# Kernel tuning notes

Hardware: AMD Instinct MI355X
Metric: run time of the kernel (lower is better)

The kernel has to match this reference:

```python
import jax, jax.numpy as jnp
import numpy as np

B, PANO, OBJ, CFG, LM, IMG, D = 64, 36, 36, 16, 8, 32, 300
H, EMB, ANG, FEAT = 512, 64, 128, 2176
TOPN = 3
EPS = 1e-8


def setup_inputs() -> dict:
    key = jax.random.key(0)
    ks = jax.random.split(key, 24)
    f = lambda i, shape: jax.random.normal(ks[i], shape, dtype=jnp.float32)
    u = lambda i, shape: jax.random.uniform(ks[i], shape, dtype=jnp.float32)
    s = 0.02
    return {
        "action": f(0, (B, ANG)),
        "feature": f(1, (B, PANO, FEAT)),
        "cand_feat": f(2, (B, IMG, FEAT)),
        "prev_h1": f(3, (B, H)),
        "c_0": f(4, (B, H)),
        "ctx": f(5, (B, CFG, H)),
        "s_0": u(6, (B, CFG)),
        "landmark_object_feature": f(7, (B, CFG, LM, D)),
        "candidate_obj_text_feat": f(8, (B, IMG, OBJ, D)),
        "landmark_mask": u(9, (B, CFG, LM)),
        "landmark_relation": f(10, (B, CFG, LM, 6)),
        "landmark_relation_mask": u(11, (B, CFG, LM)),
        "candidate_relation": f(12, (B, IMG, 6)),
        "pano_obj_feat": f(13, (B, PANO, OBJ, D)),
        "emb_W": f(14, (ANG, EMB)) * s,
        "emb_b": jnp.zeros((EMB,), jnp.float32),
        "W_ih": f(15, (EMB + FEAT + TOPN * D, 4 * H)) * s,
        "W_hh": f(16, (H, 4 * H)) * s,
        "b_lstm": jnp.zeros((4 * H,), jnp.float32),
        "feat_in_W": f(17, (H, FEAT + TOPN * D)) * s,
        "att_in_W": f(18, (H, H)) * s,
        "att_out_W": f(19, (2 * H, H)) * s,
        "cand_in_W": f(20, (H, FEAT + TOPN * 7 + TOPN * D)) * s,
        "ctx_mask": jnp.zeros((B, CFG), dtype=bool),
    }


def _cos_argmax(obj_feat, land_flat):
    # obj_feat: [B,I,O,D], land_flat: [B,M,D] -> argmax over O of cosine sim: [B,I,M]
    dot = jnp.einsum('biod,bmd->biom', obj_feat, land_flat)
    na = jnp.linalg.norm(obj_feat, axis=-1)
    nb = jnp.linalg.norm(land_flat, axis=-1)
    sim = dot / jnp.maximum(na[..., None] * nb[:, None, None, :], EPS)
    return jnp.argmax(sim, axis=2)


def reference(action, feature, cand_feat, prev_h1, c_0, ctx, s_0,
              landmark_object_feature, candidate_obj_text_feat, landmark_mask,
              landmark_relation, landmark_relation_mask, candidate_relation,
              pano_obj_feat, emb_W, emb_b, W_ih, W_hh, b_lstm, feat_in_W,
              att_in_W, att_out_W, cand_in_W, ctx_mask):
    M = CFG * LM
    land_flat = landmark_object_feature.reshape(B, M, D)

    # --- pano object retrieval (cosine argmax + top-N config*landmark gather) ---
    pano_idx = _cos_argmax(pano_obj_feat, land_flat)                   # [B,36,M]
    top_idx = jax.lax.top_k((s_0[..., None] * landmark_mask).reshape(B, M), TOPN)[1]  # [B,3]
    sel = jnp.take_along_axis(pano_idx, jnp.broadcast_to(top_idx[:, None, :], (B, PANO, TOPN)), axis=2)
    pano_sim_obj = jnp.take_along_axis(
        pano_obj_feat, jnp.broadcast_to(sel[..., None], (B, PANO, TOPN, D)), axis=2
    ).reshape(B, PANO, TOPN * D)

    # --- embed action, feature attention (dropout = identity in eval) ---
    action_embeds = jnp.tanh(action @ emb_W + emb_b)
    feat_all = jnp.concatenate([feature, pano_sim_obj], axis=-1)       # [B,36,FEAT+900]
    a = jnp.einsum('bsd,bd->bs', feat_all, prev_h1 @ feat_in_W)
    p = jax.nn.softmax(a, axis=-1)
    attn_feat = jnp.einsum('bs,bsd->bd', p, feat_all)

    # --- LSTM cell ---
    gates = jnp.concatenate([action_embeds, attn_feat], axis=-1) @ W_ih + prev_h1 @ W_hh + b_lstm
    i_g, f_g, g_g, o_g = jnp.split(gates, 4, axis=-1)
    c_1 = jax.nn.sigmoid(f_g) * c_0 + jax.nn.sigmoid(i_g) * jnp.tanh(g_g)
    h_1 = jax.nn.sigmoid(o_g) * jnp.tanh(c_1)

    # --- ctx attention with mask + tilde ---
    lg = jnp.einsum('bsd,bd->bs', ctx, h_1 @ att_in_W)
    lg = jnp.where(ctx_mask, -jnp.inf, lg)
    ctx_attn = jax.nn.softmax(lg, axis=-1)
    wctx = jnp.einsum('bs,bsd->bd', ctx_attn, ctx)
    h_tilde = jnp.tanh(jnp.concatenate([wctx, h_1], axis=-1) @ att_out_W)

    # --- candidate object retrieval ---
    cand_idx = _cos_argmax(candidate_obj_text_feat, land_flat)         # [B,IMG,M]
    ctop = jax.lax.top_k((ctx_attn[..., None] * landmark_mask).reshape(B, M), TOPN)[1]
    land_rel_top = jnp.take_along_axis(landmark_relation.reshape(B, M, 6),
                                       jnp.broadcast_to(ctop[..., None], (B, TOPN, 6)), axis=1)
    land_obj_rel = jnp.einsum('bik,bjk->bij', candidate_relation, land_rel_top)   # [B,IMG,3]
    rel_mask_top = jnp.take_along_axis(landmark_relation_mask.reshape(B, M), ctop, axis=1)  # [B,3]
    csel = jnp.take_along_axis(cand_idx, jnp.broadcast_to(ctop[:, None, :], (B, IMG, TOPN)), axis=2)
    candi_sim_obj = jnp.take_along_axis(
        candidate_obj_text_feat, jnp.broadcast_to(csel[..., None], (B, IMG, TOPN, D)), axis=2)
    candi_rel = candidate_relation[:, :, None, :] * rel_mask_top[:, None, :, None]  # [B,IMG,3,6]
    new_feat = jnp.concatenate(
        [candi_sim_obj, jnp.concatenate([candi_rel, land_obj_rel[..., None]], axis=-1)],
        axis=-1).reshape(B, IMG, TOPN * (D + 7))
    cand_all = jnp.concatenate([cand_feat, new_feat], axis=-1)

    logit = jnp.einsum('bsd,bd->bs', cand_all, h_tilde @ cand_in_W)
    return h_1, c_1, logit, h_tilde, ctx_attn
```

## Files before the change

kernel.cpp:

```cpp
#include <hip/hip_runtime.h>
#include <math.h>

#define B_    64
#define PANO_ 36
#define OBJ_  36
#define CFG_  16
#define LM_   8
#define IMG_  32
#define D_    300
#define H_    512
#define EMB_  64
#define ANG_  128
#define FEAT_ 2176
#define M_    128

__device__ __forceinline__ float sigmoidf(float x) { return 1.0f / (1.0f + expf(-x)); }
__device__ __forceinline__ float dot4(float4 a, float4 b) {
    return a.x * b.x + a.y * b.y + a.z * b.z + a.w * b.w;
}
__device__ __forceinline__ float4 add4(float4 a, float4 b) {
    return make_float4(a.x + b.x, a.y + b.y, a.z + b.z, a.w + b.w);
}
__device__ __forceinline__ float4 fma4(float s, float4 a, float4 acc) {
    return make_float4(acc.x + s * a.x, acc.y + s * a.y, acc.z + s * a.z, acc.w + s * a.w);
}
__device__ __forceinline__ float4 ld4(const float* p) { return *reinterpret_cast<const float4*>(p); }

template <int TWO_SEG, int VEC_B>
__global__ __launch_bounds__(256)
void gemm_part(const float* __restrict__ A0, int lda0, int K0, const float* __restrict__ W0,
               const float* __restrict__ A1, int lda1, int K1, const float* __restrict__ W1,
               float* __restrict__ part, int N, int kchunk) {
    __shared__ __align__(16) float As[64][36];
    __shared__ __align__(16) float Bs[32][68];
    const int K = K0 + (TWO_SEG ? K1 : 0);
    int n0 = blockIdx.x * 64;
    int k0 = blockIdx.y * kchunk;
    if (k0 >= K) return;
    int kend = min(K, k0 + kchunk);
    int tid = threadIdx.x;
    int tr = tid >> 4, tc = tid & 15;
    float4 rA4[2];
    float4 rB4[2];
    float rB[8];
    float acc[4][4] = {};

    auto loadA = [&](int kb) {
#pragma unroll
        for (int l = 0; l < 2; l++) {
            int idx = tid + 256 * l;
            int r = idx >> 3, kq = idx & 7;
            int k = kb + 4 * kq;
            float4 v = make_float4(0.f, 0.f, 0.f, 0.f);
            if (k < kend) {
                const float* src = (TWO_SEG && k >= K0)
                    ? A1 + (size_t)r * lda1 + (k - K0)
                    : A0 + (size_t)r * lda0 + k;
                v = ld4(src);
            }
            rA4[l] = v;
        }
    };
    auto loadB = [&](int kb) {
        if (VEC_B) {
#pragma unroll
            for (int l = 0; l < 2; l++) {
                int idx = tid + 256 * l;
                int kk = idx >> 4, c4 = idx & 15;
                int k = kb + kk, n = n0 + 4 * c4;
                float4 v = make_float4(0.f, 0.f, 0.f, 0.f);
                if (k < kend && n < N) {
                    const float* src = (TWO_SEG && k >= K0)
                        ? W1 + (size_t)(k - K0) * N + n
                        : W0 + (size_t)k * N + n;
                    v = ld4(src);
                }
                rB4[l] = v;
            }
        } else {
#pragma unroll
            for (int l = 0; l < 8; l++) {
                int idx = tid + 256 * l;
                int kk = idx >> 6, c = idx & 63;
                int k = kb + kk, n = n0 + c;
                float v = 0.f;
                if (k < kend && n < N) {
                    v = (TWO_SEG && k >= K0) ? W1[(size_t)(k - K0) * N + n]
                                             : W0[(size_t)k * N + n];
                }
                rB[l] = v;
            }
        }
    };
    auto storeLDS = [&]() {
#pragma unroll
        for (int l = 0; l < 2; l++) {
            int idx = tid + 256 * l;
            *reinterpret_cast<float4*>(&As[idx >> 3][4 * (idx & 7)]) = rA4[l];
        }
        if (VEC_B) {
#pragma unroll
            for (int l = 0; l < 2; l++) {
                int idx = tid + 256 * l;
                *reinterpret_cast<float4*>(&Bs[idx >> 4][4 * (idx & 15)]) = rB4[l];
            }
        } else {
#pragma unroll
            for (int l = 0; l < 8; l++) {
                int idx = tid + 256 * l;
                Bs[idx >> 6][idx & 63] = rB[l];
            }
        }
    };
    auto compute = [&]() {
#pragma unroll
        for (int kk0 = 0; kk0 < 32; kk0 += 4) {
            float4 a0 = ld4(&As[4 * tr + 0][kk0]);
            float4 a1 = ld4(&As[4 * tr + 1][kk0]);
            float4 a2 = ld4(&As[4 * tr + 2][kk0]);
            float4 a3 = ld4(&As[4 * tr + 3][kk0]);
            float4 b0 = ld4(&Bs[kk0 + 0][4 * tc]);
            float4 b1 = ld4(&Bs[kk0 + 1][4 * tc]);
            float4 b2 = ld4(&Bs[kk0 + 2][4 * tc]);
            float4 b3 = ld4(&Bs[kk0 + 3][4 * tc]);
#define ROWFMA(i, ai) \
            acc[i][0] += ai.x * b0.x + ai.y * b1.x + ai.z * b2.x + ai.w * b3.x; \
            acc[i][1] += ai.x * b0.y + ai.y * b1.y + ai.z * b2.y + ai.w * b3.y; \
            acc[i][2] += ai.x * b0.z + ai.y * b1.z + ai.z * b2.z + ai.w * b3.z; \
            acc[i][3] += ai.x * b0.w + ai.y * b1.w + ai.z * b2.w + ai.w * b3.w;
            ROWFMA(0, a0) ROWFMA(1, a1) ROWFMA(2, a2) ROWFMA(3, a3)
#undef ROWFMA
        }
    };

    loadA(k0); loadB(k0);
    storeLDS();
    __syncthreads();
    for (int kb = k0 + 32; kb < kend; kb += 32) {
        loadA(kb); loadB(kb);
        compute();
        __syncthreads();
        storeLDS();
        __syncthreads();
    }
    compute();

    float* outp = part + (size_t)blockIdx.y * 64 * N;
    if (VEC_B) {
#pragma unroll
        for (int i = 0; i < 4; i++) {
            int r = 4 * tr + i;
            int n = n0 + 4 * tc;
            if (n < N)
                *reinterpret_cast<float4*>(outp + (size_t)r * N + n) =
                    make_float4(acc[i][0], acc[i][1], acc[i][2], acc[i][3]);
        }
    } else {
#pragma unroll
        for (int i = 0; i < 4; i++) {
            int r = 4 * tr + i;
#pragma unroll
            for (int j = 0; j < 4; j++) {
                int n = n0 + 4 * tc + j;
                if (n < N) outp[(size_t)r * N + n] = acc[i][j];
            }
        }
    }
}

__global__ void reduce4_top3_kernel(const float4* __restrict__ part, int S, int total4,
                                    float4* __restrict__ out,
                                    const float* __restrict__ s0,
                                    const float* __restrict__ lmask,
                                    int* __restrict__ pmids) {
    int tid = threadIdx.x;
    if (blockIdx.x < 193) {
        int i = blockIdx.x * 256 + tid;
        if (i >= total4) return;
        float4 v = make_float4(0.f, 0.f, 0.f, 0.f);
        for (int s = 0; s < S; s++) v = add4(v, part[(size_t)s * total4 + i]);
        out[i] = v;
        return;
    }
    __shared__ float redV[2];
    __shared__ int redI[2];
    __shared__ int mids[3];
    int b = blockIdx.x - 193;
    int wave = tid >> 6, lane = tid & 63;
    float tv; int tm;
    if (tid < 128) { tv = s0[b * CFG_ + (tid >> 3)] * lmask[(size_t)b * M_ + tid]; tm = tid; }
    else { tv = -INFINITY; tm = 1 << 30; }
    for (int t = 0; t < 3; t++) {
        float bv = tv; int bi = tm;
        for (int off = 32; off >= 1; off >>= 1) {
            float ov = __shfl_xor(bv, off);
            int   oi = __shfl_xor(bi, off);
            if (ov > bv || (ov == bv && oi < bi)) { bv = ov; bi = oi; }
        }
        if (lane == 0 && wave < 2) { redV[wave] = bv; redI[wave] = bi; }
        __syncthreads();
        if (tid == 0) {
            int pick = (redV[0] > redV[1] || (redV[0] == redV[1] && redI[0] < redI[1])) ? redI[0] : redI[1];
            mids[t] = pick;
            pmids[b * 3 + t] = pick;
        }
        __syncthreads();
        if (tm == mids[t]) tv = -INFINITY;
    }
}

__global__ void reduce_remap_kernel(const float* __restrict__ part, int S,
                                    float* __restrict__ out) {
    int b = blockIdx.y;
    int c = blockIdx.x * 256 + threadIdx.x;
    if (c >= 3097) return;
    float v = 0.f;
    for (int s = 0; s < S; s++) v += part[(size_t)s * (B_ * 3097) + (size_t)b * 3097 + c];
    int oc;
    if (c < 2176) oc = c;
    else { int u = c - 2176; oc = 2176 + (u / 307) * 308 + (u % 307); }
    out[(size_t)b * 3104 + oc] = v;
}

__global__ void tanh_reduce_kernel(const float4* __restrict__ part, int S,
                                   float4* __restrict__ htld, float4* __restrict__ out_ht) {
    int i = blockIdx.x * 256 + threadIdx.x;
    if (i >= B_ * H_ / 4) return;
    float4 v = make_float4(0.f, 0.f, 0.f, 0.f);
    for (int s = 0; s < S; s++) v = add4(v, part[(size_t)s * (B_ * H_ / 4) + i]);
    float4 t = make_float4(tanhf(v.x), tanhf(v.y), tanhf(v.z), tanhf(v.w));
    htld[i] = t;
    out_ht[i] = t;
}

template <typename F>
__device__ __forceinline__ void cos_phase(int tid, const float* __restrict__ obase,
                                          const float land3[3][304], float simv[3][40],
                                          F&& dotBranch) {
    if (tid < 192) {
        int g = tid >> 2, gl = tid & 3;
        if (g < 36) {
            const float* row = obase + (size_t)g * 300;
            float c0 = 0, c1 = 0, c2 = 0, sn = 0;
            float4 buf[4];
#pragma unroll
            for (int p = 0; p < 4; p++) buf[p] = ld4(row + 4 * (gl + 4 * p));
#pragma unroll
            for (int j = 0; j < 19; j++) {
                int k4 = gl + 4 * j;
                if (k4 < 75) {
                    float4 cur = buf[j & 3];
                    int kn = gl + 4 * (j + 4);
                    if (kn < 75) buf[j & 3] = ld4(row + 4 * kn);
                    float4 l0 = ld4(&land3[0][4 * k4]);
                    float4 l1 = ld4(&land3[1][4 * k4]);
                    float4 l2 = ld4(&land3[2][4 * k4]);
                    sn += dot4(cur, cur);
                    c0 += dot4(cur, l0);
                    c1 += dot4(cur, l1);
                    c2 += dot4(cur, l2);
                }
            }
#pragma unroll
            for (int off = 1; off <= 2; off <<= 1) {
                c0 += __shfl_xor(c0, off);
                c1 += __shfl_xor(c1, off);
                c2 += __shfl_xor(c2, off);
                sn += __shfl_xor(sn, off);
            }
            if (gl == 0) {
                float inv = 1.0f / sqrtf(fmaxf(sn, 1e-20f));
                simv[0][g] = c0 * inv;
                simv[1][g] = c1 * inv;
                simv[2][g] = c2 * inv;
            }
        }
    } else {
        dotBranch(tid - 192);
    }
}

__global__ __launch_bounds__(256)
void pano_logits_kernel(const float* __restrict__ pobj,
                        const float* __restrict__ land,
                        const int* __restrict__ pmids,
                        const float* __restrict__ feature,
                        const float* __restrict__ qfeat,
                        int* __restrict__ sel,
                        float* __restrict__ aval) {
    __shared__ __align__(16) float land3[3][304];
    __shared__ int mids[3];
    __shared__ float simv[3][40];
    __shared__ int fin[3];
    __shared__ float wred[4];
    int i = blockIdx.x, b = blockIdx.y, tid = threadIdx.x;
    int wave = tid >> 6, lane = tid & 63;

    if (tid < 3) mids[tid] = pmids[b * 3 + tid];
    __syncthreads();
    for (int idx = tid; idx < 912; idx += 256) {
        int t = idx / 304, k = idx % 304;
        land3[t][k] = (k < 300) ? land[((size_t)b * 128 + mids[t]) * 300 + k] : 0.f;
    }
    __syncthreads();

    const float* obase = pobj + (((size_t)b * 36 + i) * 36) * 300;
    const float* qf = qfeat + (size_t)b * 3076;
    const float* frow = feature + ((size_t)b * 36 + i) * 2176;
    float facc = 0.f;

    cos_phase(tid, obase, land3, simv, [&](int l) {
#pragma unroll
        for (int j = 0; j < 9; j++) {
            int d4 = l + 64 * j;
            if (d4 < 544)
                facc += dot4(ld4(frow + 4 * d4), ld4(qf + 4 * d4));
        }
    });
    __syncthreads();
    if (tid < 3) {
        float bv = -INFINITY; int bo = 0;
        for (int o2 = 0; o2 < 36; o2++) {
            float v = simv[tid][o2];
            if (v > bv) { bv = v; bo = o2; }
        }
        fin[tid] = bo;
        sel[((size_t)b * 36 + i) * 3 + tid] = bo;
    }
    __syncthreads();

    float acc = facc;
    for (int idx = tid; idx < 225; idx += 256) {
        int t = idx / 75, k4 = idx % 75;
        acc += dot4(ld4(obase + (size_t)fin[t] * 300 + 4 * k4),
                    ld4(qf + 2176 + t * 300 + 4 * k4));
    }
    for (int off = 32; off >= 1; off >>= 1) acc += __shfl_xor(acc, off);
    if (lane == 0) wred[wave] = acc;
    __syncthreads();
    if (tid == 0) aval[b * 36 + i] = wred[0] + wred[1] + wred[2] + wred[3];
}

__global__ __launch_bounds__(256)
void attn_wsum_kernel(const float* __restrict__ feature,
                      const float* __restrict__ pobj,
                      const int* __restrict__ sel,
                      const float* __restrict__ aval,
                      const float* __restrict__ action,
                      const float* __restrict__ embW,
                      const float* __restrict__ embB,
                      float* __restrict__ xcat) {
    __shared__ float lg[36];
    __shared__ float pe[36];
    __shared__ int ss[36][3];
    int b = blockIdx.y, tid = threadIdx.x;
    int d4 = blockIdx.x * 256 + tid;
    if (tid < 36) lg[tid] = aval[b * 36 + tid];
    for (int idx = tid; idx < 108; idx += 256) ss[idx / 3][idx % 3] = sel[(size_t)b * 108 + idx];
    __syncthreads();
    float mx = -INFINITY;
    for (int s = 0; s < 36; s++) mx = fmaxf(mx, lg[s]);
    if (tid < 36) pe[tid] = expf(lg[tid] - mx);
    __syncthreads();
    float sum = 0;
    for (int s = 0; s < 36; s++) sum += pe[s];
    float invS = 1.0f / sum;
    if (d4 < 769) {
        float4 acc = make_float4(0.f, 0.f, 0.f, 0.f);
        if (d4 < 544) {
            const float* fb = feature + (size_t)b * 36 * 2176 + 4 * d4;
#pragma unroll 4
            for (int s = 0; s < 36; s++) acc = fma4(pe[s], ld4(fb + (size_t)s * 2176), acc);
        } else {
            int u = d4 - 544, t = u / 75, k4 = u % 75;
            const float* pb = pobj + (size_t)b * 36 * 36 * 300;
#pragma unroll 4
            for (int s = 0; s < 36; s++)
                acc = fma4(pe[s], ld4(pb + ((size_t)s * 36 + ss[s][t]) * 300 + 4 * k4), acc);
        }
        acc = make_float4(acc.x * invS, acc.y * invS, acc.z * invS, acc.w * invS);
        *reinterpret_cast<float4*>(xcat + (size_t)b * 3140 + 64 + 4 * d4) = acc;
    }
    if (blockIdx.x == 0 && tid < 64) {
        float acc = embB[tid];
        for (int k = 0; k < ANG_; k++)
            acc += action[b * ANG_ + k] * embW[k * EMB_ + tid];
        xcat[(size_t)b * 3140 + tid] = tanhf(acc);
    }
}

__global__ void lstm_kernel(const float* __restrict__ gp, int S,
                            const float* __restrict__ b_lstm,
                            const float* __restrict__ c0,
                            float* __restrict__ out_h1,
                            float* __restrict__ out_c1) {
    int idx4 = blockIdx.x * 256 + threadIdx.x;
    if (idx4 >= B_ * H_ / 4) return;
    int b = idx4 >> 7;
    int d4 = idx4 & 127;
    float4 ig = ld4(b_lstm + 4 * d4);
    float4 fg = ld4(b_lstm + 512 + 4 * d4);
    float4 gg = ld4(b_lstm + 1024 + 4 * d4);
    float4 og = ld4(b_lstm + 1536 + 4 * d4);
    for (int s = 0; s < S; s++) {
        const float* g = gp + (size_t)s * (B_ * 2048) + (size_t)b * 2048 + 4 * d4;
        ig = add4(ig, ld4(g));
        fg = add4(fg, ld4(g + 512));
        gg = add4(gg, ld4(g + 1024));
        og = add4(og, ld4(g + 1536));
    }
    float4 cv = ld4(c0 + 4 * idx4);
    float4 c1, h1;
    c1.x = sigmoidf(fg.x) * cv.x + sigmoidf(ig.x) * tanhf(gg.x);
    c1.y = sigmoidf(fg.y) * cv.y + sigmoidf(ig.y) * tanhf(gg.y);
    c1.z = sigmoidf(fg.z) * cv.z + sigmoidf(ig.z) * tanhf(gg.z);
    c1.w = sigmoidf(fg.w) * cv.w + sigmoidf(ig.w) * tanhf(gg.w);
    h1.x = sigmoidf(og.x) * tanhf(c1.x);
    h1.y = sigmoidf(og.y) * tanhf(c1.y);
    h1.z = sigmoidf(og.z) * tanhf(c1.z);
    h1.w = sigmoidf(og.w) * tanhf(c1.w);
    *reinterpret_cast<float4*>(out_c1 + 4 * idx4) = c1;
    *reinterpret_cast<float4*>(out_h1 + 4 * idx4) = h1;
}

__global__ __launch_bounds__(256)
void ctx_attn_kernel(const float* __restrict__ ctx,
                     const float* __restrict__ qctx_part,
                     const float* __restrict__ h1f,
                     const float* __restrict__ lmask,
                     float* __restrict__ ccbuf,
                     float* __restrict__ out_attn,
                     int* __restrict__ ctop) {
    __shared__ __align__(16) float qc[512];
    __shared__ float part[16][17];
    __shared__ float lgv[16];
    __shared__ float att[16];
    __shared__ float redV[2];
    __shared__ int redI[2];
    __shared__ int mids[3];
    int b = blockIdx.x, tid = threadIdx.x;
    int wave = tid >> 6, lane = tid & 63;
    if (tid < 128) {
        float4 v = make_float4(0.f, 0.f, 0.f, 0.f);
#pragma unroll
        for (int s = 0; s < 8; s++)
            v = add4(v, ld4(qctx_part + (size_t)s * (B_ * 512) + (size_t)b * 512 + 4 * tid));
        *reinterpret_cast<float4*>(&qc[4 * tid]) = v;
    }
    __syncthreads();
    int s = tid >> 4, l = tid & 15;
    float acc = 0;
    for (int d = l; d < 512; d += 16) acc += ctx[((size_t)b * 16 + s) * 512 + d] * qc[d];
    part[s][l] = acc;
    __syncthreads();
    if (tid < 16) {
        float sum = 0;
        for (int j = 0; j < 16; j++) sum += part[tid][j];
        lgv[tid] = sum;
    }
    __syncthreads();
    if (tid < 16) {
        float mx = -INFINITY;
        for (int j = 0; j < 16; j++) mx = fmaxf(mx, lgv[j]);
        att[tid] = expf(lgv[tid] - mx);
    }
    __syncthreads();
    float sum = 0;
    for (int j = 0; j < 16; j++) sum += att[j];
    float invS = 1.0f / sum;
    if (tid < 16) out_attn[b * 16 + tid] = att[tid] * invS;
    for (int d = tid; d < 512; d += 256) {
        float acc2 = 0;
        for (int sj = 0; sj < 16; sj++)
            acc2 += att[sj] * ctx[((size_t)b * 16 + sj) * 512 + d];
        ccbuf[(size_t)b * 1024 + d] = acc2 * invS;
        ccbuf[(size_t)b * 1024 + 512 + d] = h1f[(size_t)b * 512 + d];
    }
    float tv; int tm;
    if (tid < 128) { tv = att[tid >> 3] * lmask[(size_t)b * M_ + tid]; tm = tid; }
    else { tv = -INFINITY; tm = 1 << 30; }
    for (int t = 0; t < 3; t++) {
        float bv = tv; int bi = tm;
        for (int off = 32; off >= 1; off >>= 1) {
            float ov = __shfl_xor(bv, off);
            int   oi = __shfl_xor(bi, off);
            if (ov > bv || (ov == bv && oi < bi)) { bv = ov; bi = oi; }
        }
        if (lane == 0 && wave < 2) { redV[wave] = bv; redI[wave] = bi; }
        __syncthreads();
        if (tid == 0) {
            int pick = (redV[0] > redV[1] || (redV[0] == redV[1] && redI[0] < redI[1])) ? redI[0] : redI[1];
            mids[t] = pick;
            ctop[b * 3 + t] = pick;
        }
        __syncthreads();
        if (tm == mids[t]) tv = -INFINITY;
    }
}

__global__ __launch_bounds__(256)
void cand_fused_kernel(const float* __restrict__ cobj,
                       const float* __restrict__ land,
                       const int* __restrict__ ctop,
                       const float* __restrict__ landrel,
                       const float* __restrict__ lrmask,
                       const float* __restrict__ crel_g,
                       const float* __restrict__ cand_feat,
                       const float* __restrict__ qcand,
                       float* __restrict__ out_logit) {
    __shared__ __align__(16) float land3[3][304];
    __shared__ float relL[3][6];
    __shared__ float relM[3];
    __shared__ float crel[6];
    __shared__ int mids[3];
    __shared__ float simv[3][40];
    __shared__ int fin[3];
    __shared__ float wsum[4];
    int img = blockIdx.x, b = blockIdx.y, tid = threadIdx.x;
    int wave = tid >> 6, lane = tid & 63;
    if (tid < 3) mids[tid] = ctop[b * 3 + tid];
    __syncthreads();
    for (int idx = tid; idx < 912; idx += 256) {
        int t = idx / 304, k = idx % 304;
        land3[t][k] = (k < 300) ? land[((size_t)b * 128 + mids[t]) * 300 + k] : 0.f;
    }
    if (tid < 18) { int t = tid / 6, k = tid % 6; relL[t][k] = landrel[((size_t)b * 128 + mids[t]) * 6 + k]; }
    if (tid >= 32 && tid < 35) { int t = tid - 32; relM[t] = lrmask[(size_t)b * 128 + mids[t]]; }
    if (tid >= 64 && tid < 70) { crel[tid - 64] = crel_g[((size_t)b * 32 + img) * 6 + (tid - 64)]; }
    __syncthreads();

    const float* obase = cobj + (((size_t)b * 32 + img) * 36) * 300;
    const float* q = qcand + (size_t)b * 3104;
    const float* cf = cand_feat + ((size_t)b * 32 + img) * 2176;
    float facc = 0.f;

    cos_phase(tid, obase, land3, simv, [&](int l) {
#pragma unroll
        for (int j = 0; j < 9; j++) {
            int d4 = l + 64 * j;
            if (d4 < 544)
                facc += dot4(ld4(cf + 4 * d4), ld4(q + 4 * d4));
        }
    });
    __syncthreads();
    if (tid < 3) {
        float bv = -INFINITY; int bo = 0;
        for (int o2 = 0; o2 < 36; o2++) {
            float v = simv[tid][o2];
            if (v > bv) { bv = v; bo = o2; }
        }
        fin[tid] = bo;
    }
    __syncthreads();

    float acc = facc;
    for (int idx = tid; idx < 225; idx += 256) {
        int t = idx / 75, k4 = idx % 75;
        acc += dot4(ld4(obase + (size_t)fin[t] * 300 + 4 * k4),
                    ld4(q + 2176 + t * 308 + 4 * k4));
    }
    if (tid < 21) {
        int t = tid / 7, j = tid % 7;
        float val;
        if (j < 6) val = crel[j] * relM[t];
        else { val = 0; for (int k = 0; k < 6; k++) val += crel[k] * relL[t][k]; }
        acc += val * q[2176 + t * 308 + 300 + j];
    }
    for (int off = 32; off >= 1; off >>= 1) acc += __shfl_xor(acc, off);
    if (lane == 0) wsum[wave] = acc;
    __syncthreads();
    if (tid == 0) {
        out_logit[(size_t)b * 32 + img] = wsum[0] + wsum[1] + wsum[2] + wsum[3];
    }
}

extern "C" void kernel_launch(void* const* d_in, const int* in_sizes, int n_in,
                              void* d_out, int out_size, void* d_ws, size_t ws_size,
                              hipStream_t stream) {
    const float* action    = (const float*)d_in[0];
    const float* feature   = (const float*)d_in[1];
    const float* cand_feat = (const float*)d_in[2];
    const float* prev_h1   = (const float*)d_in[3];
    const float* c_0       = (const float*)d_in[4];
    const float* ctx       = (const float*)d_in[5];
    const float* s_0       = (const float*)d_in[6];
    const float* lobj      = (const float*)d_in[7];
    const float* cobj      = (const float*)d_in[8];
    const float* lmask     = (const float*)d_in[9];
    const float* lrel      = (const float*)d_in[10];
    const float* lrelmask  = (const float*)d_in[11];
    const float* crel      = (const float*)d_in[12];
    const float* pobj      = (const float*)d_in[13];
    const float* embW      = (const float*)d_in[14];
    const float* embB      = (const float*)d_in[15];
    const float* W_ih      = (const float*)d_in[16];
    const float* W_hh      = (const float*)d_in[17];
    const float* b_lstm    = (const float*)d_in[18];
    const float* feat_in_W = (const float*)d_in[19];
    const float* att_in_W  = (const float*)d_in[20];
    const float* att_out_W = (const float*)d_in[21];
    const float* cand_in_W = (const float*)d_in[22];

    float* ws = (float*)d_ws;
    float* gates_part = ws;
    float* qf_part    = gates_part + 2621440;
    float* q_feat     = qf_part + 1574912;
    float* qctx_part  = q_feat + 196864;
    float* htpre_part = qctx_part + 262144;
    float* htld       = htpre_part + 524288;
    float* qcand_part = htld + 32768;
    float* q_cand     = qcand_part + 1585664;
    float* xcat       = q_cand + 198656;
    float* ccbuf      = xcat + 200960;
    float* aval       = ccbuf + 65536;
    int*   ctop       = (int*)(aval + 2304);
    int*   sel        = ctop + 192;
    int*   pmids      = sel + 6912;

    float* out       = (float*)d_out;
    float* out_h1    = out;
    float* out_c1    = out + 32768;
    float* out_logit = out + 65536;
    float* out_ht    = out + 67584;
    float* out_attn  = out + 100352;

    gemm_part<0, 1><<<dim3(49, 8), 256, 0, stream>>>(prev_h1, H_, H_, feat_in_W,
                                                     nullptr, 0, 0, nullptr,
                                                     qf_part, 3076, 64);
    reduce4_top3_kernel<<<257, 256, 0, stream>>>((const float4*)qf_part, 8, 49216,
                                                 (float4*)q_feat, s_0, lmask, pmids);

    pano_logits_kernel<<<dim3(PANO_, B_), 256, 0, stream>>>(pobj, lobj, pmids, feature, q_feat, sel, aval);

    attn_wsum_kernel<<<dim3(4, B_), 256, 0, stream>>>(feature, pobj, sel, aval, action, embW, embB, xcat);

    gemm_part<1, 1><<<dim3(32, 20), 256, 0, stream>>>(xcat, 3140, 3140, W_ih,
                                                      prev_h1, H_, H_, W_hh,
                                                      gates_part, 2048, 192);
    lstm_kernel<<<32, 256, 0, stream>>>(gates_part, 20, b_lstm, c_0, out_h1, out_c1);

    gemm_part<0, 1><<<dim3(8, 8), 256, 0, stream>>>(out_h1, H_, H_, att_in_W,
                                                    nullptr, 0, 0, nullptr,
                                                    qctx_part, H_, 64);
    ctx_attn_kernel<<<B_, 256, 0, stream>>>(ctx, qctx_part, out_h1, lmask, ccbuf, out_attn, ctop);

    gemm_part<0, 1><<<dim3(8, 16), 256, 0, stream>>>(ccbuf, 1024, 1024, att_out_W,
                                                     nullptr, 0, 0, nullptr,
                                                     htpre_part, H_, 64);
    tanh_reduce_kernel<<<32, 256, 0, stream>>>((const float4*)htpre_part, 16,
                                               (float4*)htld, (float4*)out_ht);

    gemm_part<0, 0><<<dim3(49, 8), 256, 0, stream>>>(htld, H_, H_, cand_in_W,
                                                     nullptr, 0, 0, nullptr,
                                                     qcand_part, 3097, 64);
    reduce_remap_kernel<<<dim3(13, B_), 256, 0, stream>>>(qcand_part, 8, q_cand);

    cand_fused_kernel<<<dim3(IMG_, B_), 256, 0, stream>>>(cobj, lobj, ctop, lrel, lrelmask,
                                                          crel, cand_feat, q_cand, out_logit);
}
```

Measured before the change: 488.8 us.

## Stage object tile in shared memory with coalesced loads for cosine argmax

Both the pano and candidate logit kernels now copy the whole 36x300 object-feature block into a padded shared-memory tile using all threads with coalesced float4 loads. The cosine similarity and the later gather of the selected objects then read from LDS instead of global memory. The feature dot product that used to overlap in the spare warp is moved after the argmax and spread across all threads. The roughly 44 KB of LDS per block may reduce occupancy, and the feature loads are no longer overlapped with the cosine phase.

```diff
diff --git a/kernel.cpp b/kernel.cpp
--- a/kernel.cpp
+++ b/kernel.cpp
@@ -233,53 +233,6 @@
     out_ht[i] = t;
 }
 
-template <typename F>
-__device__ __forceinline__ void cos_phase(int tid, const float* __restrict__ obase,
-                                          const float land3[3][304], float simv[3][40],
-                                          F&& dotBranch) {
-    if (tid < 192) {
-        int g = tid >> 2, gl = tid & 3;
-        if (g < 36) {
-            const float* row = obase + (size_t)g * 300;
-            float c0 = 0, c1 = 0, c2 = 0, sn = 0;
-            float4 buf[4];
-#pragma unroll
-            for (int p = 0; p < 4; p++) buf[p] = ld4(row + 4 * (gl + 4 * p));
-#pragma unroll
-            for (int j = 0; j < 19; j++) {
-                int k4 = gl + 4 * j;
-                if (k4 < 75) {
-                    float4 cur = buf[j & 3];
-                    int kn = gl + 4 * (j + 4);
-                    if (kn < 75) buf[j & 3] = ld4(row + 4 * kn);
-                    float4 l0 = ld4(&land3[0][4 * k4]);
-                    float4 l1 = ld4(&land3[1][4 * k4]);
-                    float4 l2 = ld4(&land3[2][4 * k4]);
-                    sn += dot4(cur, cur);
-                    c0 += dot4(cur, l0);
-                    c1 += dot4(cur, l1);
-                    c2 += dot4(cur, l2);
-                }
-            }
-#pragma unroll
-            for (int off = 1; off <= 2; off <<= 1) {
-                c0 += __shfl_xor(c0, off);
-                c1 += __shfl_xor(c1, off);
-                c2 += __shfl_xor(c2, off);
-                sn += __shfl_xor(sn, off);
-            }
-            if (gl == 0) {
-                float inv = 1.0f / sqrtf(fmaxf(sn, 1e-20f));
-                simv[0][g] = c0 * inv;
-                simv[1][g] = c1 * inv;
-                simv[2][g] = c2 * inv;
-            }
-        }
-    } else {
-        dotBranch(tid - 192);
-    }
-}
-
 __global__ __launch_bounds__(256)
 void pano_logits_kernel(const float* __restrict__ pobj,
                         const float* __restrict__ land,
@@ -288,6 +241,7 @@
                         const float* __restrict__ qfeat,
                         int* __restrict__ sel,
                         float* __restrict__ aval) {
+    __shared__ __align__(16) float tile[36][308];
     __shared__ __align__(16) float land3[3][304];
     __shared__ int mids[3];
     __shared__ float simv[3][40];
@@ -298,25 +252,43 @@
 
     if (tid < 3) mids[tid] = pmids[b * 3 + tid];
     __syncthreads();
-    for (int idx = tid; idx < 912; idx += 256) {
-        int t = idx / 304, k = idx % 304;
-        land3[t][k] = (k < 300) ? land[((size_t)b * 128 + mids[t]) * 300 + k] : 0.f;
-    }
-    __syncthreads();
-
+
+    for (int q = tid; q < 225; q += 256) {
+        int t = q / 75, k4 = q % 75;
+        *reinterpret_cast<float4*>(&land3[t][4 * k4]) =
+            ld4(land + ((size_t)b * 128 + mids[t]) * 300 + 4 * k4);
+    }
     const float* obase = pobj + (((size_t)b * 36 + i) * 36) * 300;
-    const float* qf = qfeat + (size_t)b * 3076;
-    const float* frow = feature + ((size_t)b * 36 + i) * 2176;
-    float facc = 0.f;
-
-    cos_phase(tid, obase, land3, simv, [&](int l) {
-#pragma unroll
-        for (int j = 0; j < 9; j++) {
-            int d4 = l + 64 * j;
-            if (d4 < 544)
-                facc += dot4(ld4(frow + 4 * d4), ld4(qf + 4 * d4));
-        }
-    });
+    for (int q = tid; q < 2700; q += 256) {
+        int o = q / 75, k4 = q % 75;
+        *reinterpret_cast<float4*>(&tile[o][4 * k4]) = ld4(obase + (size_t)o * 300 + 4 * k4);
+    }
+    __syncthreads();
+
+    int g = tid >> 2, gl = tid & 3;
+    if (g < 36) {
+        float c0 = 0, c1 = 0, c2 = 0, sn = 0;
+        for (int k4 = gl; k4 < 75; k4 += 4) {
+            float4 a = ld4(&tile[g][4 * k4]);
+            sn += dot4(a, a);
+            c0 += dot4(a, ld4(&land3[0][4 * k4]));
+            c1 += dot4(a, ld4(&land3[1][4 * k4]));
+            c2 += dot4(a, ld4(&land3[2][4 * k4]));
+        }
+#pragma unroll
+        for (int off = 1; off <= 2; off <<= 1) {
+            c0 += __shfl_xor(c0, off);
+            c1 += __shfl_xor(c1, off);
+            c2 += __shfl_xor(c2, off);
+            sn += __shfl_xor(sn, off);
+        }
+        if (gl == 0) {
+            float inv = 1.0f / sqrtf(fmaxf(sn, 1e-20f));
+            simv[0][g] = c0 * inv;
+            simv[1][g] = c1 * inv;
+            simv[2][g] = c2 * inv;
+        }
+    }
     __syncthreads();
     if (tid < 3) {
         float bv = -INFINITY; int bo = 0;
@@ -329,11 +301,14 @@
     }
     __syncthreads();
 
-    float acc = facc;
-    for (int idx = tid; idx < 225; idx += 256) {
-        int t = idx / 75, k4 = idx % 75;
-        acc += dot4(ld4(obase + (size_t)fin[t] * 300 + 4 * k4),
-                    ld4(qf + 2176 + t * 300 + 4 * k4));
+    const float* qf = qfeat + (size_t)b * 3076;
+    const float* frow = feature + ((size_t)b * 36 + i) * 2176;
+    float acc = 0;
+    for (int d4 = tid; d4 < 544; d4 += 256)
+        acc += dot4(ld4(frow + 4 * d4), ld4(qf + 4 * d4));
+    for (int q = tid; q < 225; q += 256) {
+        int t = q / 75, k4 = q % 75;
+        acc += dot4(ld4(&tile[fin[t]][4 * k4]), ld4(qf + 2176 + t * 300 + 4 * k4));
     }
     for (int off = 32; off >= 1; off >>= 1) acc += __shfl_xor(acc, off);
     if (lane == 0) wred[wave] = acc;
@@ -508,6 +483,7 @@
                        const float* __restrict__ cand_feat,
                        const float* __restrict__ qcand,
                        float* __restrict__ out_logit) {
+    __shared__ __align__(16) float tile[36][308];
     __shared__ __align__(16) float land3[3][304];
     __shared__ float relL[3][6];
     __shared__ float relM[3];
@@ -520,28 +496,46 @@
     int wave = tid >> 6, lane = tid & 63;
     if (tid < 3) mids[tid] = ctop[b * 3 + tid];
     __syncthreads();
-    for (int idx = tid; idx < 912; idx += 256) {
-        int t = idx / 304, k = idx % 304;
-        land3[t][k] = (k < 300) ? land[((size_t)b * 128 + mids[t]) * 300 + k] : 0.f;
+
+    for (int q = tid; q < 225; q += 256) {
+        int t = q / 75, k4 = q % 75;
+        *reinterpret_cast<float4*>(&land3[t][4 * k4]) =
+            ld4(land + ((size_t)b * 128 + mids[t]) * 300 + 4 * k4);
+    }
+    const float* obase = cobj + (((size_t)b * 32 + img) * 36) * 300;
+    for (int q = tid; q < 2700; q += 256) {
+        int o = q / 75, k4 = q % 75;
+        *reinterpret_cast<float4*>(&tile[o][4 * k4]) = ld4(obase + (size_t)o * 300 + 4 * k4);
     }
     if (tid < 18) { int t = tid / 6, k = tid % 6; relL[t][k] = landrel[((size_t)b * 128 + mids[t]) * 6 + k]; }
     if (tid >= 32 && tid < 35) { int t = tid - 32; relM[t] = lrmask[(size_t)b * 128 + mids[t]]; }
     if (tid >= 64 && tid < 70) { crel[tid - 64] = crel_g[((size_t)b * 32 + img) * 6 + (tid - 64)]; }
     __syncthreads();
 
-    const float* obase = cobj + (((size_t)b * 32 + img) * 36) * 300;
-    const float* q = qcand + (size_t)b * 3104;
-    const float* cf = cand_feat + ((size_t)b * 32 + img) * 2176;
-    float facc = 0.f;
-
-    cos_phase(tid, obase, land3, simv, [&](int l) {
-#pragma unroll
-        for (int j = 0; j < 9; j++) {
-            int d4 = l + 64 * j;
-            if (d4 < 544)
-                facc += dot4(ld4(cf + 4 * d4), ld4(q + 4 * d4));
-        }
-    });
+    int g = tid >> 2, gl = tid & 3;
+    if (g < 36) {
+        float c0 = 0, c1 = 0, c2 = 0, sn = 0;
+        for (int k4 = gl; k4 < 75; k4 += 4) {
+            float4 a = ld4(&tile[g][4 * k4]);
+            sn += dot4(a, a);
+            c0 += dot4(a, ld4(&land3[0][4 * k4]));
+            c1 += dot4(a, ld4(&land3[1][4 * k4]));
+            c2 += dot4(a, ld4(&land3[2][4 * k4]));
+        }
+#pragma unroll
+        for (int off = 1; off <= 2; off <<= 1) {
+            c0 += __shfl_xor(c0, off);
+            c1 += __shfl_xor(c1, off);
+            c2 += __shfl_xor(c2, off);
+            sn += __shfl_xor(sn, off);
+        }
+        if (gl == 0) {
+            float inv = 1.0f / sqrtf(fmaxf(sn, 1e-20f));
+            simv[0][g] = c0 * inv;
+            simv[1][g] = c1 * inv;
+            simv[2][g] = c2 * inv;
+        }
+    }
     __syncthreads();
     if (tid < 3) {
         float bv = -INFINITY; int bo = 0;
@@ -553,11 +547,14 @@
     }
     __syncthreads();
 
-    float acc = facc;
-    for (int idx = tid; idx < 225; idx += 256) {
-        int t = idx / 75, k4 = idx % 75;
-        acc += dot4(ld4(obase + (size_t)fin[t] * 300 + 4 * k4),
-                    ld4(q + 2176 + t * 308 + 4 * k4));
+    const float* q = qcand + (size_t)b * 3104;
+    const float* cf = cand_feat + ((size_t)b * 32 + img) * 2176;
+    float acc = 0;
+    for (int d4 = tid; d4 < 544; d4 += 256)
+        acc += dot4(ld4(cf + 4 * d4), ld4(q + 4 * d4));
+    for (int qq = tid; qq < 225; qq += 256) {
+        int t = qq / 75, k4 = qq % 75;
+        acc += dot4(ld4(&tile[fin[t]][4 * k4]), ld4(q + 2176 + t * 308 + 4 * k4));
     }
     if (tid < 21) {
         int t = tid / 7, j = tid % 7;
```

Result: faster. 445.5 us (-8.9%).
